# Kernel optimization log

Hardware: AMD Instinct MI355X
Metric: run time of the kernel (lower is better)

## Reference

```python
import jax, jax.numpy as jnp
import numpy as np

N_NODES = 32767   # complete binary tree, depth 15
EMB_DIM = 256
HIDDEN = 256      # 'hidden_size' -> LSTM state is 2*HIDDEN
VOCAB = 32        # len(ExprNode.TYPE_LIST)


def setup_inputs() -> dict:
    key = jax.random.key(0)
    k1, k2, k3, k4, k5, k6 = jax.random.split(key, 6)
    H2 = 2 * HIDDEN
    types = jax.random.randint(k1, (N_NODES,), 0, VOCAB, dtype=jnp.int32)
    # complete binary tree: children of node i are 2i+1 / 2i+2; sentinel slot N = zero state
    idx = np.arange(N_NODES)
    a = 2 * idx + 1
    b = 2 * idx + 2
    a = np.where(a < N_NODES, a, N_NODES).astype(np.int32)
    b = np.where(b < N_NODES, b, N_NODES).astype(np.int32)
    scale = 1.0 / np.sqrt(H2)
    return {
        "types": types,
        "a_idx": jnp.asarray(a),
        "b_idx": jnp.asarray(b),
        "emb": jax.random.normal(k2, (VOCAB, EMB_DIM), jnp.float32) * 0.02,
        "W_ih": jax.random.normal(k3, (4 * H2, EMB_DIM), jnp.float32) * scale,
        "W_hh": jax.random.normal(k4, (4 * H2, H2), jnp.float32) * scale,
        "b_ih": jax.random.normal(k5, (4 * H2,), jnp.float32) * scale,
        "b_hh": jax.random.normal(k6, (4 * H2,), jnp.float32) * scale,
    }


def reference(types, a_idx, b_idx, emb, W_ih, W_hh, b_ih, b_hh):
    """Recursive binary tree-LSTM over topological (leaves-first) order.
    Each node's LSTM state has size 2H; a parent's incoming (h, c) is the concat
    of the first H entries of each child's state (zeros for missing children).
    Returns per-node hidden outputs [N, 2H] (the out_map, indexed by node id)."""
    N = types.shape[0]
    H2 = W_hh.shape[1]
    H = H2 // 2
    # batched input projection for all nodes at once: [N, 4*H2]
    x_proj = emb[types] @ W_ih.T + (b_ih + b_hh)
    Hs0 = jnp.zeros((N + 1, H2), x_proj.dtype)  # slot N = h0 (zeros)
    Cs0 = jnp.zeros((N + 1, H2), x_proj.dtype)
    order = jnp.arange(N - 1, -1, -1)  # children (higher index) before parents

    def step(carry, i):
        Hs, Cs = carry
        h = jnp.concatenate([Hs[a_idx[i], :H], Hs[b_idx[i], :H]])  # [2H]
        c = jnp.concatenate([Cs[a_idx[i], :H], Cs[b_idx[i], :H]])
        gates = x_proj[i] + W_hh @ h                 # [4*H2], torch gate order i,f,g,o
        ig, fg, gg, og = jnp.split(gates, 4)
        c_new = jax.nn.sigmoid(fg) * c + jax.nn.sigmoid(ig) * jnp.tanh(gg)
        h_new = jax.nn.sigmoid(og) * jnp.tanh(c_new)
        return (Hs.at[i].set(h_new), Cs.at[i].set(c_new)), h_new

    _, outs = jax.lax.scan(step, (Hs0, Cs0), order)
    return outs[::-1]  # reorder so row i is node i's output
```

## Files before the change

kernel.cpp:

```cpp
#include <hip/hip_runtime.h>
#include <hip/hip_bf16.h>


#define NNODES 32767

typedef __attribute__((ext_vector_type(8))) short bf16x8;
typedef __attribute__((ext_vector_type(4))) float f32x4;

__device__ __forceinline__ float sigf(float x) { return 1.0f / (1.0f + __expf(-x)); }
__device__ __forceinline__ float tanhfast(float x) { return 2.0f / (1.0f + __expf(-2.0f * x)) - 1.0f; }

__device__ __forceinline__ short bf_hi(float x) {
    __hip_bfloat16 h = __float2bfloat16(x);
    return __builtin_bit_cast(short, h);
}
__device__ __forceinline__ float bf_f(short s) {
    __hip_bfloat16 h = __builtin_bit_cast(__hip_bfloat16, s);
    return __bfloat162float(h);
}
__device__ __forceinline__ void split8(const float* src, short* hi, short* lo) {
#pragma unroll
    for (int j = 0; j < 8; ++j) {
        float x = src[j];
        short h = bf_hi(x);
        hi[j] = h;
        lo[j] = bf_hi(x - bf_f(h));
    }
}

__global__ void proj_kernel(const float* __restrict__ emb, const float* __restrict__ W_ih,
                            const float* __restrict__ b_ih, const float* __restrict__ b_hh,
                            float* __restrict__ proj) {
    __shared__ float e[256];
    int v = blockIdx.x >> 3;
    int rc = blockIdx.x & 7;
    int t = threadIdx.x;
    e[t] = emb[v * 256 + t];
    __syncthreads();
    int r = rc * 256 + t;
    const float4* w4 = (const float4*)(W_ih + (size_t)r * 256);
    const float4* e4 = (const float4*)e;
    float acc = 0.f;
#pragma unroll 8
    for (int k = 0; k < 64; ++k) {
        float4 w = w4[k];
        float4 h = e4[k];
        acc += w.x * h.x + w.y * h.y + w.z * h.z + w.w * h.w;
    }
    proj[v * 2048 + r] = acc + b_ih[r] + b_hh[r];
}

__global__ void wpack_kernel(const float* __restrict__ W_hh,
                             short* __restrict__ Whi, short* __restrict__ Wlo) {
    int t = blockIdx.x * 256 + threadIdx.x;
    int lane = t & 63;
    int kt = (t >> 6) & 15;
    int ntile = t >> 10;
    int n = ntile * 16 + (lane & 15);
    int k0 = kt * 32 + (lane >> 4) * 8;
    const float* src = W_hh + (size_t)n * 512 + k0;
    short hi[8], lo[8];
    split8(src, hi, lo);
    *(bf16x8*)(Whi + (size_t)t * 8) = *(bf16x8*)hi;
    *(bf16x8*)(Wlo + (size_t)t * 8) = *(bf16x8*)lo;
}

__global__ void leaf_kernel(const int* __restrict__ types, const float* __restrict__ proj,
                            float* __restrict__ out, float* __restrict__ C256,
                            short* __restrict__ Hsplit) {
    int bi = blockIdx.x;
    int node = 16383 + (bi >> 1);
    int j = ((bi & 1) << 8) + threadIdx.x;
    int tt = types[node];
    const float* p = proj + (size_t)tt * 2048;
    float gi = p[j];
    float gg = p[1024 + j];
    float go = p[1536 + j];
    float cn = sigf(gi) * tanhfast(gg);
    float hn = sigf(go) * tanhfast(cn);
    out[(size_t)node * 512 + j] = hn;
    if ((bi & 1) == 0) {
        C256[(size_t)node * 256 + j] = cn;
        short hi = bf_hi(hn);
        Hsplit[(size_t)node * 512 + j] = hi;
        Hsplit[(size_t)node * 512 + 256 + j] = bf_hi(hn - bf_f(hi));
    }
}

__global__ __launch_bounds__(256) void gemm_lstm_kernel(
    const int* __restrict__ a_idx, const int* __restrict__ b_idx,
    const int* __restrict__ types, float* __restrict__ out,
    const short* __restrict__ Whi, const short* __restrict__ Wlo,
    const float* __restrict__ proj, float* __restrict__ C256,
    short* __restrict__ Hsplit, int node_base, int Jc) {
    __shared__ short Ahi[2][16][64][8];
    __shared__ short Alo[2][16][64][8];
    __shared__ int sA[32], sB[32], sT[32];
    int t = threadIdx.x;
    int node0 = node_base + blockIdx.x * 32;
    if (t < 32) {
        sA[t] = a_idx[node0 + t];
        sB[t] = b_idx[node0 + t];
        sT[t] = types[node0 + t];
    }
    __syncthreads();

#pragma unroll
    for (int it = 0; it < 8; ++it) {
        int c = it * 256 + t;
        int mt = c >> 10;
        int kt = (c >> 6) & 15;
        int lane = c & 63;
        int m_loc = mt * 16 + (lane & 15);
        int k0 = kt * 32 + (lane >> 4) * 8;
        int child = (k0 < 256) ? sA[m_loc] : sB[m_loc];
        const short* src = Hsplit + (size_t)child * 512 + (k0 & 255);
        *(bf16x8*)&Ahi[mt][kt][lane][0] = *(const bf16x8*)src;
        *(bf16x8*)&Alo[mt][kt][lane][0] = *(const bf16x8*)(src + 256);
    }
    __syncthreads();

    int w = t >> 6;
    int lane = t & 63;
    int jsteps = Jc >> 4;
    int jbase = blockIdx.y * Jc;

    auto epilogue = [&](int j0, f32x4 (&acc)[4][2]) {
        int j = j0 + (lane & 15);
        int jc = j & 255;
        bool fh = (j < 256);
#pragma unroll
        for (int mt = 0; mt < 2; ++mt) {
            int mrow = mt * 16 + (lane >> 4) * 4;
#pragma unroll
            for (int r = 0; r < 4; ++r) {
                int m_loc = mrow + r;
                int node = node0 + m_loc;
                const float* p = proj + (size_t)sT[m_loc] * 2048 + j;
                float gi = acc[0][mt][r] + p[0];
                float gf = acc[1][mt][r] + p[512];
                float gg = acc[2][mt][r] + p[1024];
                float go = acc[3][mt][r] + p[1536];
                int child = fh ? sA[m_loc] : sB[m_loc];
                float c = C256[(size_t)child * 256 + jc];
                float cn = sigf(gf) * c + sigf(gi) * tanhfast(gg);
                float hn = sigf(go) * tanhfast(cn);
                out[(size_t)node * 512 + j] = hn;
                if (fh) {
                    C256[(size_t)node * 256 + j] = cn;
                    short hi = bf_hi(hn);
                    Hsplit[(size_t)node * 512 + j] = hi;
                    Hsplit[(size_t)node * 512 + 256 + j] = bf_hi(hn - bf_f(hi));
                }
            }
        }
    };

    if (jsteps >= 4) {
        for (int js = w; js < jsteps; js += 4) {
            int j0 = jbase + js * 16;
            f32x4 acc[4][2];
#pragma unroll
            for (int q = 0; q < 4; ++q)
#pragma unroll
                for (int mt = 0; mt < 2; ++mt) acc[q][mt] = (f32x4){0.f, 0.f, 0.f, 0.f};
            int nt0 = j0 >> 4;
#pragma unroll 4
            for (int kt = 0; kt < 16; ++kt) {
                bf16x8 ah0 = *(const bf16x8*)&Ahi[0][kt][lane][0];
                bf16x8 al0 = *(const bf16x8*)&Alo[0][kt][lane][0];
                bf16x8 ah1 = *(const bf16x8*)&Ahi[1][kt][lane][0];
                bf16x8 al1 = *(const bf16x8*)&Alo[1][kt][lane][0];
#pragma unroll
                for (int q = 0; q < 4; ++q) {
                    int ntile = q * 32 + nt0;
                    size_t off = ((size_t)(ntile * 16 + kt) * 64 + lane) * 8;
                    bf16x8 bh = *(const bf16x8*)(Whi + off);
                    bf16x8 bl = *(const bf16x8*)(Wlo + off);
                    acc[q][0] = __builtin_amdgcn_mfma_f32_16x16x32_bf16(ah0, bh, acc[q][0], 0, 0, 0);
                    acc[q][0] = __builtin_amdgcn_mfma_f32_16x16x32_bf16(ah0, bl, acc[q][0], 0, 0, 0);
                    acc[q][0] = __builtin_amdgcn_mfma_f32_16x16x32_bf16(al0, bh, acc[q][0], 0, 0, 0);
                    acc[q][1] = __builtin_amdgcn_mfma_f32_16x16x32_bf16(ah1, bh, acc[q][1], 0, 0, 0);
                    acc[q][1] = __builtin_amdgcn_mfma_f32_16x16x32_bf16(ah1, bl, acc[q][1], 0, 0, 0);
                    acc[q][1] = __builtin_amdgcn_mfma_f32_16x16x32_bf16(al1, bh, acc[q][1], 0, 0, 0);
                }
            }
            epilogue(j0, acc);
        }
    } else {
        int js = w & 1;
        int khalf = w >> 1;
        int j0 = jbase + js * 16;
        f32x4 acc[4][2];
#pragma unroll
        for (int q = 0; q < 4; ++q)
#pragma unroll
            for (int mt = 0; mt < 2; ++mt) acc[q][mt] = (f32x4){0.f, 0.f, 0.f, 0.f};
        int nt0 = j0 >> 4;
        int kt0 = khalf * 8;
#pragma unroll 4
        for (int kt = kt0; kt < kt0 + 8; ++kt) {
            bf16x8 ah0 = *(const bf16x8*)&Ahi[0][kt][lane][0];
            bf16x8 al0 = *(const bf16x8*)&Alo[0][kt][lane][0];
            bf16x8 ah1 = *(const bf16x8*)&Ahi[1][kt][lane][0];
            bf16x8 al1 = *(const bf16x8*)&Alo[1][kt][lane][0];
#pragma unroll
            for (int q = 0; q < 4; ++q) {
                int ntile = q * 32 + nt0;
                size_t off = ((size_t)(ntile * 16 + kt) * 64 + lane) * 8;
                bf16x8 bh = *(const bf16x8*)(Whi + off);
                bf16x8 bl = *(const bf16x8*)(Wlo + off);
                acc[q][0] = __builtin_amdgcn_mfma_f32_16x16x32_bf16(ah0, bh, acc[q][0], 0, 0, 0);
                acc[q][0] = __builtin_amdgcn_mfma_f32_16x16x32_bf16(ah0, bl, acc[q][0], 0, 0, 0);
                acc[q][0] = __builtin_amdgcn_mfma_f32_16x16x32_bf16(al0, bh, acc[q][0], 0, 0, 0);
                acc[q][1] = __builtin_amdgcn_mfma_f32_16x16x32_bf16(ah1, bh, acc[q][1], 0, 0, 0);
                acc[q][1] = __builtin_amdgcn_mfma_f32_16x16x32_bf16(ah1, bl, acc[q][1], 0, 0, 0);
                acc[q][1] = __builtin_amdgcn_mfma_f32_16x16x32_bf16(al1, bh, acc[q][1], 0, 0, 0);
            }
        }
        __syncthreads();
        float* xch = (float*)&Ahi[0][0][0][0];
        if (khalf == 1) {
#pragma unroll
            for (int q = 0; q < 4; ++q)
#pragma unroll
                for (int mt = 0; mt < 2; ++mt)
                    *(f32x4*)&xch[(((q * 2 + mt) * 128) + js * 64 + lane) * 4] = acc[q][mt];
        }
        __syncthreads();
        if (khalf == 0) {
#pragma unroll
            for (int q = 0; q < 4; ++q)
#pragma unroll
                for (int mt = 0; mt < 2; ++mt) {
                    f32x4 o = *(const f32x4*)&xch[(((q * 2 + mt) * 128) + js * 64 + lane) * 4];
                    acc[q][mt] += o;
                }
            epilogue(j0, acc);
        }
    }
}

__global__ void small_gemm_kernel(
    const int* __restrict__ a_idx, const int* __restrict__ b_idx,
    const float* __restrict__ out, const float* __restrict__ W_hh,
    float* __restrict__ part, int node_base) {
    __shared__ float hs[64];
    int t = threadIdx.x;
    int n = blockIdx.x;
    int node = node_base + n;
    int kbase = blockIdx.z * 64;
    if (t < 16) {
        int child = (kbase < 256) ? a_idx[node] : b_idx[node];
        float4 v = ((const float4*)(out + (size_t)child * 512 + (kbase & 255)))[t];
        ((float4*)hs)[t] = v;
    }
    __syncthreads();
    int r = blockIdx.y * 256 + t;
    const float4* w4 = (const float4*)(W_hh + (size_t)r * 512 + kbase);
    const float4* h4 = (const float4*)hs;
    float acc = 0.f;
#pragma unroll
    for (int k = 0; k < 16; ++k) {
        float4 wv = w4[k];
        float4 hv = h4[k];
        acc += wv.x * hv.x + wv.y * hv.y + wv.z * hv.z + wv.w * hv.w;
    }
    part[((size_t)blockIdx.z * gridDim.x + n) * 2048 + r] = acc;
}

__global__ void small_combine_kernel(
    const int* __restrict__ a_idx, const int* __restrict__ b_idx,
    const int* __restrict__ types, const float* __restrict__ part,
    const float* __restrict__ proj, float* __restrict__ C256,
    short* __restrict__ Hsplit, float* __restrict__ out, int node_base, int B) {
    int bi = blockIdx.x;
    int n = bi >> 1;
    int j = ((bi & 1) << 8) + threadIdx.x;
    int node = node_base + n;
    float g[4] = {0.f, 0.f, 0.f, 0.f};
    for (int z = 0; z < 8; ++z) {
        const float* p = part + ((size_t)z * B + n) * 2048;
#pragma unroll
        for (int q = 0; q < 4; ++q) g[q] += p[q * 512 + j];
    }
    const float* p = proj + (size_t)types[node] * 2048 + j;
    float gi = g[0] + p[0];
    float gf = g[1] + p[512];
    float gg = g[2] + p[1024];
    float go = g[3] + p[1536];
    int child = (j < 256) ? a_idx[node] : b_idx[node];
    float c = C256[(size_t)child * 256 + (j & 255)];
    float cn = sigf(gf) * c + sigf(gi) * tanhfast(gg);
    float hn = sigf(go) * tanhfast(cn);
    out[(size_t)node * 512 + j] = hn;
    if (j < 256) {
        C256[(size_t)node * 256 + j] = cn;
        short hi = bf_hi(hn);
        Hsplit[(size_t)node * 512 + j] = hi;
        Hsplit[(size_t)node * 512 + 256 + j] = bf_hi(hn - bf_f(hi));
    }
}

extern "C" void kernel_launch(void* const* d_in, const int* in_sizes, int n_in,
                              void* d_out, int out_size, void* d_ws, size_t ws_size,
                              hipStream_t stream) {
    const int* types = (const int*)d_in[0];
    const int* a_idx = (const int*)d_in[1];
    const int* b_idx = (const int*)d_in[2];
    const float* emb = (const float*)d_in[3];
    const float* W_ih = (const float*)d_in[4];
    const float* W_hh = (const float*)d_in[5];
    const float* b_ih = (const float*)d_in[6];
    const float* b_hh = (const float*)d_in[7];
    float* out = (float*)d_out;

    float* ws = (float*)d_ws;
    float* proj = ws;
    float* C256 = ws + 65536;
    short* Hsplit = (short*)(C256 + 8388352);
    short* Whi = Hsplit + 16777216;
    short* Wlo = Whi + 1048576;
    float* part = (float*)(Wlo + 1048576);

    proj_kernel<<<256, 256, 0, stream>>>(emb, W_ih, b_ih, b_hh, proj);
    wpack_kernel<<<512, 256, 0, stream>>>(W_hh, Whi, Wlo);
    leaf_kernel<<<32768, 256, 0, stream>>>(types, proj, out, C256, Hsplit);

    for (int d = 13; d >= 0; --d) {
        int base = (1 << d) - 1;
        int B = 1 << d;
        if (B >= 32) {
            int bx = B / 32;
            int J = 2;
            while (bx * J < 512 && J < 16) J <<= 1;
            gemm_lstm_kernel<<<dim3(bx, J), 256, 0, stream>>>(
                a_idx, b_idx, types, out, Whi, Wlo, proj, C256, Hsplit, base, 512 / J);
        } else {
            small_gemm_kernel<<<dim3(B, 8, 8), 256, 0, stream>>>(
                a_idx, b_idx, out, W_hh, part, base);
            small_combine_kernel<<<B * 2, 256, 0, stream>>>(
                a_idx, b_idx, types, part, proj, C256, Hsplit, out, base, B);
        }
    }
}
```

Baseline: 460.0 us.

## Add 128-node tiled MFMA kernel with async LDS loads for wide tree levels

Adds a new GEMM+LSTM kernel for tree levels with at least 1024 nodes. Each block handles 128 nodes by 32 hidden columns across all four gates. It stages the gathered child states and the packed weights into double-buffered shared memory through global_load_lds, then runs three-term split-bf16 MFMAs and fuses the LSTM cell update into the epilogue. The larger tile is meant to raise weight and activation reuse and overlap loads with compute on the large levels. The cost is heavier per-block LDS use and a fixed tile shape that only fits levels whose node count is a multiple of 128.

```diff
diff --git a/kernel.cpp b/kernel.cpp
--- a/kernel.cpp
+++ b/kernel.cpp
@@ -6,6 +6,9 @@
 
 typedef __attribute__((ext_vector_type(8))) short bf16x8;
 typedef __attribute__((ext_vector_type(4))) float f32x4;
+
+typedef const __attribute__((address_space(1))) void* gptr_t;
+typedef __attribute__((address_space(3))) void* lptr_t;
 
 __device__ __forceinline__ float sigf(float x) { return 1.0f / (1.0f + __expf(-x)); }
 __device__ __forceinline__ float tanhfast(float x) { return 2.0f / (1.0f + __expf(-2.0f * x)) - 1.0f; }
@@ -84,6 +87,139 @@
         short hi = bf_hi(hn);
         Hsplit[(size_t)node * 512 + j] = hi;
         Hsplit[(size_t)node * 512 + 256 + j] = bf_hi(hn - bf_f(hi));
+    }
+}
+
+__global__ __launch_bounds__(256) void big_gemm_lstm_kernel(
+    const int* __restrict__ a_idx, const int* __restrict__ b_idx,
+    const int* __restrict__ types, float* __restrict__ out,
+    const short* __restrict__ Whi,
+    const float* __restrict__ proj, float* __restrict__ C256,
+    short* __restrict__ Hsplit, int node_base) {
+    __shared__ __align__(16) short lds[2][16384];
+    __shared__ int sA[128], sB[128], sT[128];
+
+    int t = threadIdx.x;
+    int lin = blockIdx.x;
+    int x = lin >> 4;
+    int y = (lin & 7) * 2 + ((lin >> 3) & 1);
+    int node0 = node_base + x * 128;
+    int j0 = y * 32;
+
+    if (t < 128) {
+        sA[t] = a_idx[node0 + t];
+        sB[t] = b_idx[node0 + t];
+        sT[t] = types[node0 + t];
+    }
+    __syncthreads();
+
+    int w = t >> 6, lane = t & 63;
+    int wm = w >> 1, wn = w & 1;
+
+    unsigned b0[8], b1[8];
+    const short* tbl;
+    unsigned stepk;
+    if (w < 2) {
+        tbl = Hsplit;
+        stepk = 32;
+#pragma unroll
+        for (int i = 0; i < 8; ++i) {
+            int c = w * 8 + i;
+            int mt = c >> 1, part = c & 1;
+            int m_loc = mt * 16 + (lane & 15);
+            unsigned ks = (unsigned)part * 256u + (unsigned)(lane >> 4) * 8u;
+            b0[i] = (unsigned)sA[m_loc] * 512u + ks;
+            b1[i] = (unsigned)sB[m_loc] * 512u + ks;
+        }
+    } else {
+        tbl = Whi;
+        stepk = 512;
+#pragma unroll
+        for (int i = 0; i < 8; ++i) {
+            int cc = (w - 2) * 8 + i;
+            int nt = cc >> 1, part = cc & 1;
+            int q = nt >> 1, sub = nt & 1;
+            unsigned ntg = (unsigned)(q * 32 + y * 2 + sub);
+            b0[i] = ntg * 8192u + (unsigned)part * 1048576u + (unsigned)lane * 8u;
+            b1[i] = b0[i] + 4096u;
+        }
+    }
+
+    f32x4 acc[4][4];
+#pragma unroll
+    for (int i = 0; i < 4; ++i)
+#pragma unroll
+        for (int q = 0; q < 4; ++q) acc[i][q] = (f32x4){0.f, 0.f, 0.f, 0.f};
+
+    auto stage = [&](int kt, int buf) {
+#pragma unroll
+        for (int i = 0; i < 8; ++i) {
+            unsigned off = ((kt < 8) ? b0[i] : b1[i]) + (unsigned)(kt & 7) * stepk;
+            const short* gsrc = tbl + off;
+            short* ldst = &lds[buf][(w * 8 + i) * 512];
+            __builtin_amdgcn_global_load_lds((gptr_t)gsrc, (lptr_t)ldst, 16, 0, 0);
+        }
+    };
+
+    auto compute = [&](int buf) {
+        const short* L = lds[buf];
+        bf16x8 ah[4], al[4];
+#pragma unroll
+        for (int i = 0; i < 4; ++i) {
+            int mt = wm * 4 + i;
+            ah[i] = *(const bf16x8*)&L[(mt * 2) * 512 + lane * 8];
+            al[i] = *(const bf16x8*)&L[(mt * 2 + 1) * 512 + lane * 8];
+        }
+#pragma unroll
+        for (int q = 0; q < 4; ++q) {
+            int nt = q * 2 + wn;
+            bf16x8 bh = *(const bf16x8*)&L[(16 + nt * 2) * 512 + lane * 8];
+            bf16x8 bl = *(const bf16x8*)&L[(17 + nt * 2) * 512 + lane * 8];
+#pragma unroll
+            for (int i = 0; i < 4; ++i) {
+                acc[i][q] = __builtin_amdgcn_mfma_f32_16x16x32_bf16(ah[i], bh, acc[i][q], 0, 0, 0);
+                acc[i][q] = __builtin_amdgcn_mfma_f32_16x16x32_bf16(ah[i], bl, acc[i][q], 0, 0, 0);
+                acc[i][q] = __builtin_amdgcn_mfma_f32_16x16x32_bf16(al[i], bh, acc[i][q], 0, 0, 0);
+            }
+        }
+    };
+
+    stage(0, 0);
+    __syncthreads();
+    for (int kt = 0; kt < 16; ++kt) {
+        int cur = kt & 1;
+        if (kt < 15) stage(kt + 1, cur ^ 1);
+        compute(cur);
+        __syncthreads();
+    }
+
+    int j = j0 + wn * 16 + (lane & 15);
+    bool fh = (j < 256);
+    int jc = j & 255;
+#pragma unroll
+    for (int i = 0; i < 4; ++i) {
+        int mrow = wm * 64 + i * 16 + (lane >> 4) * 4;
+#pragma unroll
+        for (int r = 0; r < 4; ++r) {
+            int m_loc = mrow + r;
+            int node = node0 + m_loc;
+            const float* p = proj + (size_t)sT[m_loc] * 2048 + j;
+            float gi = acc[i][0][r] + p[0];
+            float gf = acc[i][1][r] + p[512];
+            float gg = acc[i][2][r] + p[1024];
+            float go = acc[i][3][r] + p[1536];
+            int child = fh ? sA[m_loc] : sB[m_loc];
+            float c = C256[(size_t)child * 256 + jc];
+            float cn = sigf(gf) * c + sigf(gi) * tanhfast(gg);
+            float hn = sigf(go) * tanhfast(cn);
+            out[(size_t)node * 512 + j] = hn;
+            if (fh) {
+                C256[(size_t)node * 256 + j] = cn;
+                short hi = bf_hi(hn);
+                Hsplit[(size_t)node * 512 + j] = hi;
+                Hsplit[(size_t)node * 512 + 256 + j] = bf_hi(hn - bf_f(hi));
+            }
+        }
     }
 }
 
@@ -330,7 +466,11 @@
     for (int d = 13; d >= 0; --d) {
         int base = (1 << d) - 1;
         int B = 1 << d;
-        if (B >= 32) {
+        if (B >= 1024) {
+            int X = B / 128;
+            big_gemm_lstm_kernel<<<X * 16, 256, 0, stream>>>(
+                a_idx, b_idx, types, out, Whi, proj, C256, Hsplit, base);
+        } else if (B >= 32) {
             int bx = B / 32;
             int J = 2;
             while (bx * J < 512 && J < 16) J <<= 1;
```

Measured after the change: 418.4 us. 9.1% less time.
